# Performance work log

Hardware: AMD Instinct MI355X
Metric: run time of the kernel (lower is better)

Reference implementation:

```python
import jax, jax.numpy as jnp
import numpy as np
from jax import lax

C_RED = 32
IN_CH = 256
BN_EPS = 1e-5
NORM_EPS = 1e-6


def setup_inputs() -> dict:
    key = jax.random.key(0)
    ks = jax.random.split(key, 5)
    B, H, W = 16, 64, 64
    x = jax.random.normal(ks[0], (B, IN_CH, H, W), dtype=jnp.float32)
    w_reduce = jax.random.normal(ks[1], (C_RED, IN_CH), dtype=jnp.float32) * 0.05
    bn_gamma = jnp.ones((C_RED,), dtype=jnp.float32)
    bn_beta = jnp.zeros((C_RED,), dtype=jnp.float32)
    bn_mean = jax.random.normal(ks[2], (C_RED,), dtype=jnp.float32) * 0.1
    bn_var = jax.random.uniform(ks[3], (C_RED,), dtype=jnp.float32, minval=0.5, maxval=1.5)
    # depthwise 3x3 kernel, OIHW with I=1 (groups == channels)
    dw_weight = jax.random.normal(ks[4], (C_RED, 1, 3, 3), dtype=jnp.float32) * 0.1
    scale = jnp.ones((C_RED,), dtype=jnp.float32)
    return {"x": x, "w_reduce": w_reduce, "bn_gamma": bn_gamma, "bn_beta": bn_beta,
            "bn_mean": bn_mean, "bn_var": bn_var, "dw_weight": dw_weight, "scale": scale}


def _l2_normalize(t):
    # F.normalize(p=2, dim=1, eps=1e-6): divide by max(||t||_2, eps) along channel dim
    n = jnp.sqrt(jnp.sum(t * t, axis=1, keepdims=True))
    return t / jnp.maximum(n, NORM_EPS)


def reference(x, w_reduce, bn_gamma, bn_beta, bn_mean, bn_var, dw_weight, scale):
    # 1x1 reduce conv (no bias)
    z = jnp.einsum('bihw,oi->bohw', x, w_reduce)
    # BatchNorm2d (inference: running stats)
    inv = bn_gamma / jnp.sqrt(bn_var + BN_EPS)
    z = z * inv[None, :, None, None] + (bn_beta - bn_mean * inv)[None, :, None, None]
    z = jax.nn.relu(z)
    # SpiralTwist: depthwise 3x3 conv (SAME) then per-channel scale
    z_tw = lax.conv_general_dilated(
        z, dw_weight, window_strides=(1, 1), padding='SAME',
        feature_group_count=C_RED,
        dimension_numbers=('NCHW', 'OIHW', 'NCHW'))
    z_tw = z_tw * scale[None, :, None, None]
    z_norm = _l2_normalize(z)
    z_tw_norm = _l2_normalize(z_tw)
    # upper-triangular channel pairs (i <= j)
    idx_i, idx_j = np.triu_indices(C_RED, k=0)
    pair = z_norm[:, idx_i] * z_tw_norm[:, idx_j]  # [B, C*(C+1)/2, H, W]
    return jnp.concatenate([z_norm, pair], axis=1)
```

## Files before the change

kernel.cpp:

```cpp
#include <hip/hip_runtime.h>
#include <hip/hip_bf16.h>
#include <stdint.h>

#define HW   4096
#define CIN  256
#define CR   32
#define COUT 560

__global__ __launch_bounds__(256) void k_conv1x1(
    const float* __restrict__ x,
    const float* __restrict__ wr,
    const float* __restrict__ gamma,
    const float* __restrict__ beta,
    const float* __restrict__ mean,
    const float* __restrict__ var,
    float* __restrict__ z)
{
    const int tid = threadIdx.x;
    const int og  = __builtin_amdgcn_readfirstlane(tid >> 6);
    const int g0  = blockIdx.x * 64 + (tid & 63);
    const int b   = g0 >> 12;
    const int p   = g0 & 4095;

    const float* xb = x + ((((size_t)b) * CIN) << 12) + p;
    const float* wp = wr + (size_t)og * 8 * CIN;

    float acc[8] = {0.f,0.f,0.f,0.f,0.f,0.f,0.f,0.f};

    for (int cc = 0; cc < 16; ++cc) {
        float xv[16];
        #pragma unroll
        for (int k = 0; k < 16; ++k)
            xv[k] = xb[((size_t)(cc * 16 + k)) << 12];
        #pragma unroll
        for (int o = 0; o < 8; ++o) {
            #pragma unroll
            for (int k = 0; k < 16; ++k)
                acc[o] = fmaf(xv[k], wp[o * CIN + cc * 16 + k], acc[o]);
        }
    }

    #pragma unroll
    for (int o = 0; o < 8; ++o) {
        const int oc = og * 8 + o;
        const float inv = gamma[oc] / sqrtf(var[oc] + 1e-5f);
        const float bia = beta[oc] - mean[oc] * inv;
        z[((((size_t)b) * CR + oc) << 12) + p] =
            fmaxf(fmaf(acc[o], inv, bia), 0.f);
    }
}

__global__ __launch_bounds__(256) void k_twist(
    const float* __restrict__ z,
    const float* __restrict__ dww,
    const float* __restrict__ scl,
    float* __restrict__ out)
{
    __shared__ float dml[CR * 9];
    __shared__ float sc[CR];
    __shared__ float ps1[4 * 64];
    __shared__ float ps2[4 * 64];
    __shared__ float znl[CR * 64];
    __shared__ float twl[CR * 64];

    const int tid = threadIdx.x;
    for (int t = tid; t < CR * 9; t += 256) dml[t] = dww[t];
    if (tid < CR) sc[tid] = scl[tid];
    __syncthreads();

    const int cg  = __builtin_amdgcn_readfirstlane(tid >> 6);
    const int px  = tid & 63;
    const int g0  = blockIdx.x * 64;
    const int b   = g0 >> 12;
    const int p0  = g0 & 4095;
    const int h   = p0 >> 6;
    const float* zb = z + (((size_t)b * CR) << 12);

    float zc[8], tw[8];
    float s1 = 0.f, s2 = 0.f;
    #pragma unroll
    for (int k = 0; k < 8; ++k) {
        const int c = cg * 8 + k;
        const float* zp = zb + ((size_t)c << 12);
        float acc = 0.f, center = 0.f;
        #pragma unroll
        for (int dy = 0; dy < 3; ++dy) {
            const int hy = h + dy - 1;
            const bool rok = ((unsigned)hy) < 64u;
            #pragma unroll
            for (int dx = 0; dx < 3; ++dx) {
                const int wx = px + dx - 1;
                const bool ok = rok && (((unsigned)wx) < 64u);
                float v = 0.f;
                if (ok) v = zp[(hy << 6) + wx];
                if (dy == 1 && dx == 1) center = v;
                acc = fmaf(v, dml[c * 9 + dy * 3 + dx], acc);
            }
        }
        const float t = acc * sc[c];
        zc[k] = center; tw[k] = t;
        s1 = fmaf(center, center, s1);
        s2 = fmaf(t, t, s2);
    }
    ps1[cg * 64 + px] = s1;
    ps2[cg * 64 + px] = s2;
    __syncthreads();
    const float t1 = ps1[px] + ps1[64 + px] + ps1[128 + px] + ps1[192 + px];
    const float t2 = ps2[px] + ps2[64 + px] + ps2[128 + px] + ps2[192 + px];
    const float rn1 = 1.0f / fmaxf(sqrtf(t1), 1e-6f);
    const float rn2 = 1.0f / fmaxf(sqrtf(t2), 1e-6f);
    #pragma unroll
    for (int k = 0; k < 8; ++k) {
        znl[(cg * 8 + k) * 64 + px] = zc[k] * rn1;
        twl[(cg * 8 + k) * 64 + px] = tw[k] * rn2;
    }
    __syncthreads();

    float* outb = out + (((size_t)b * COUT) << 12) + p0 + px;
    #pragma unroll
    for (int P = 0; P < 32; ++P)
        if ((P & 3) == cg)
            outb[(size_t)P << 12] = znl[P * 64 + px];
    {
        int P = 32;
        #pragma unroll
        for (int i = 0; i < CR; ++i) {
            #pragma unroll
            for (int j = i; j < CR; ++j) {
                if ((P & 3) == cg)
                    outb[(size_t)P << 12] = znl[i * 64 + px] * twl[j * 64 + px];
                ++P;
            }
        }
    }
}

extern "C" void kernel_launch(void* const* d_in, const int* in_sizes, int n_in,
                              void* d_out, int out_size, void* d_ws, size_t ws_size,
                              hipStream_t stream) {
    const float* x     = (const float*)d_in[0];
    const float* wr    = (const float*)d_in[1];
    const float* gamma = (const float*)d_in[2];
    const float* beta  = (const float*)d_in[3];
    const float* mean  = (const float*)d_in[4];
    const float* var   = (const float*)d_in[5];
    const float* dww   = (const float*)d_in[6];
    const float* scl   = (const float*)d_in[7];
    float* z = (float*)d_ws;
    float* out = (float*)d_out;

    hipLaunchKernelGGL(k_conv1x1, dim3(1024), dim3(256), 0, stream,
                       x, wr, gamma, beta, mean, var, z);
    hipLaunchKernelGGL(k_twist, dim3(1024), dim3(256), 0, stream,
                       z, dww, scl, out);
}
```

Baseline: 240.0 us.

## Fuse 1x1 conv, BN-ReLU and depthwise twist into one kernel with halo recompute

Merges the reduce-conv kernel and the twist/pair kernel into a single kernel where each block owns one image row and recomputes the 1x1 conv for the rows above and below to form the 3x3 halo. This removes the round trip of the intermediate z tensor through global memory and one launch. It triples the conv arithmetic and input reads per block. The normalized values are also cached in registers for the pair products instead of rereading shared memory.

```diff
diff --git a/kernel.cpp b/kernel.cpp
--- a/kernel.cpp
+++ b/kernel.cpp
@@ -1,134 +1,141 @@
 #include <hip/hip_runtime.h>
-#include <hip/hip_bf16.h>
 #include <stdint.h>
 
-#define HW   4096
 #define CIN  256
 #define CR   32
 #define COUT 560
 
-__global__ __launch_bounds__(256) void k_conv1x1(
+__global__ __launch_bounds__(256, 4) void k_fused(
     const float* __restrict__ x,
     const float* __restrict__ wr,
     const float* __restrict__ gamma,
     const float* __restrict__ beta,
     const float* __restrict__ mean,
     const float* __restrict__ var,
-    float* __restrict__ z)
-{
-    const int tid = threadIdx.x;
-    const int og  = __builtin_amdgcn_readfirstlane(tid >> 6);
-    const int g0  = blockIdx.x * 64 + (tid & 63);
-    const int b   = g0 >> 12;
-    const int p   = g0 & 4095;
-
-    const float* xb = x + ((((size_t)b) * CIN) << 12) + p;
-    const float* wp = wr + (size_t)og * 8 * CIN;
-
-    float acc[8] = {0.f,0.f,0.f,0.f,0.f,0.f,0.f,0.f};
-
-    for (int cc = 0; cc < 16; ++cc) {
-        float xv[16];
-        #pragma unroll
-        for (int k = 0; k < 16; ++k)
-            xv[k] = xb[((size_t)(cc * 16 + k)) << 12];
-        #pragma unroll
-        for (int o = 0; o < 8; ++o) {
-            #pragma unroll
-            for (int k = 0; k < 16; ++k)
-                acc[o] = fmaf(xv[k], wp[o * CIN + cc * 16 + k], acc[o]);
-        }
-    }
-
-    #pragma unroll
-    for (int o = 0; o < 8; ++o) {
-        const int oc = og * 8 + o;
-        const float inv = gamma[oc] / sqrtf(var[oc] + 1e-5f);
-        const float bia = beta[oc] - mean[oc] * inv;
-        z[((((size_t)b) * CR + oc) << 12) + p] =
-            fmaxf(fmaf(acc[o], inv, bia), 0.f);
-    }
-}
-
-__global__ __launch_bounds__(256) void k_twist(
-    const float* __restrict__ z,
     const float* __restrict__ dww,
     const float* __restrict__ scl,
     float* __restrict__ out)
 {
+    __shared__ float buf[3 * CR * 64];
+    __shared__ float ps1[4 * 64], ps2[4 * 64];
     __shared__ float dml[CR * 9];
     __shared__ float sc[CR];
-    __shared__ float ps1[4 * 64];
-    __shared__ float ps2[4 * 64];
-    __shared__ float znl[CR * 64];
-    __shared__ float twl[CR * 64];
 
     const int tid = threadIdx.x;
     for (int t = tid; t < CR * 9; t += 256) dml[t] = dww[t];
     if (tid < CR) sc[tid] = scl[tid];
+
+    const int cg = __builtin_amdgcn_readfirstlane(tid >> 6);
+    const int px = tid & 63;
+    const int g  = blockIdx.x;
+    const int b  = g >> 6;
+    const int h  = g & 63;
+    const int ob = cg * 8;
+
+    float acc[3][8];
+    #pragma unroll
+    for (int r = 0; r < 3; ++r)
+        #pragma unroll
+        for (int o = 0; o < 8; ++o) acc[r][o] = 0.f;
+
+    const float* xb = x + (((size_t)b * CIN) << 12) + px;
+    const int hc0 = (h == 0)  ? 0  : h - 1;
+    const int hc2 = (h == 63) ? 63 : h + 1;
+
+    #pragma unroll 2
+    for (int c0 = 0; c0 < CIN; c0 += 8) {
+        float xv[8][3];
+        #pragma unroll
+        for (int k = 0; k < 8; ++k) {
+            const float* xp = xb + ((size_t)(c0 + k) << 12);
+            xv[k][0] = xp[hc0 << 6];
+            xv[k][1] = xp[h   << 6];
+            xv[k][2] = xp[hc2 << 6];
+        }
+        #pragma unroll
+        for (int o = 0; o < 8; ++o) {
+            const float* wp = wr + (ob + o) * CIN + c0;
+            #pragma unroll
+            for (int k = 0; k < 8; ++k) {
+                const float wv = wp[k];
+                acc[0][o] = fmaf(xv[k][0], wv, acc[0][o]);
+                acc[1][o] = fmaf(xv[k][1], wv, acc[1][o]);
+                acc[2][o] = fmaf(xv[k][2], wv, acc[2][o]);
+            }
+        }
+    }
+
+    const bool v0 = (h > 0), v2 = (h < 63);
+    float zrow[3][8];
+    #pragma unroll
+    for (int o = 0; o < 8; ++o) {
+        const int oc = ob + o;
+        const float inv = gamma[oc] / sqrtf(var[oc] + 1e-5f);
+        const float bia = beta[oc] - mean[oc] * inv;
+        zrow[0][o] = v0 ? fmaxf(fmaf(acc[0][o], inv, bia), 0.f) : 0.f;
+        zrow[1][o] =      fmaxf(fmaf(acc[1][o], inv, bia), 0.f);
+        zrow[2][o] = v2 ? fmaxf(fmaf(acc[2][o], inv, bia), 0.f) : 0.f;
+    }
+    #pragma unroll
+    for (int r = 0; r < 3; ++r)
+        #pragma unroll
+        for (int o = 0; o < 8; ++o)
+            buf[((r * CR) + ob + o) * 64 + px] = zrow[r][o];
     __syncthreads();
 
-    const int cg  = __builtin_amdgcn_readfirstlane(tid >> 6);
-    const int px  = tid & 63;
-    const int g0  = blockIdx.x * 64;
-    const int b   = g0 >> 12;
-    const int p0  = g0 & 4095;
-    const int h   = p0 >> 6;
-    const float* zb = z + (((size_t)b * CR) << 12);
-
-    float zc[8], tw[8];
+    float twv[8], zcv[8];
     float s1 = 0.f, s2 = 0.f;
     #pragma unroll
     for (int k = 0; k < 8; ++k) {
-        const int c = cg * 8 + k;
-        const float* zp = zb + ((size_t)c << 12);
-        float acc = 0.f, center = 0.f;
+        const int c = ob + k;
+        float a = 0.f;
         #pragma unroll
-        for (int dy = 0; dy < 3; ++dy) {
-            const int hy = h + dy - 1;
-            const bool rok = ((unsigned)hy) < 64u;
-            #pragma unroll
-            for (int dx = 0; dx < 3; ++dx) {
-                const int wx = px + dx - 1;
-                const bool ok = rok && (((unsigned)wx) < 64u);
-                float v = 0.f;
-                if (ok) v = zp[(hy << 6) + wx];
-                if (dy == 1 && dx == 1) center = v;
-                acc = fmaf(v, dml[c * 9 + dy * 3 + dx], acc);
-            }
+        for (int r = 0; r < 3; ++r) {
+            const float* zp = &buf[(r * CR + c) * 64];
+            const float vL = (px > 0)  ? zp[px - 1] : 0.f;
+            const float vC =             zp[px];
+            const float vR = (px < 63) ? zp[px + 1] : 0.f;
+            a = fmaf(vL, dml[c * 9 + r * 3 + 0], a);
+            a = fmaf(vC, dml[c * 9 + r * 3 + 1], a);
+            a = fmaf(vR, dml[c * 9 + r * 3 + 2], a);
         }
-        const float t = acc * sc[c];
-        zc[k] = center; tw[k] = t;
-        s1 = fmaf(center, center, s1);
+        const float t = a * sc[c];
+        twv[k] = t;
+        zcv[k] = zrow[1][k];
+        s1 = fmaf(zcv[k], zcv[k], s1);
         s2 = fmaf(t, t, s2);
     }
     ps1[cg * 64 + px] = s1;
     ps2[cg * 64 + px] = s2;
     __syncthreads();
-    const float t1 = ps1[px] + ps1[64 + px] + ps1[128 + px] + ps1[192 + px];
-    const float t2 = ps2[px] + ps2[64 + px] + ps2[128 + px] + ps2[192 + px];
-    const float rn1 = 1.0f / fmaxf(sqrtf(t1), 1e-6f);
-    const float rn2 = 1.0f / fmaxf(sqrtf(t2), 1e-6f);
+    const float rn1 = 1.f / fmaxf(sqrtf(ps1[px] + ps1[64 + px] + ps1[128 + px] + ps1[192 + px]), 1e-6f);
+    const float rn2 = 1.f / fmaxf(sqrtf(ps2[px] + ps2[64 + px] + ps2[128 + px] + ps2[192 + px]), 1e-6f);
+
     #pragma unroll
     for (int k = 0; k < 8; ++k) {
-        znl[(cg * 8 + k) * 64 + px] = zc[k] * rn1;
-        twl[(cg * 8 + k) * 64 + px] = tw[k] * rn2;
+        buf[(ob + k) * 64 + px]        = zcv[k] * rn1;
+        buf[2048 + (ob + k) * 64 + px] = twv[k] * rn2;
     }
     __syncthreads();
 
-    float* outb = out + (((size_t)b * COUT) << 12) + p0 + px;
+    float zn[CR], tw[CR];
     #pragma unroll
-    for (int P = 0; P < 32; ++P)
-        if ((P & 3) == cg)
-            outb[(size_t)P << 12] = znl[P * 64 + px];
+    for (int c = 0; c < CR; ++c) {
+        zn[c] = buf[c * 64 + px];
+        tw[c] = buf[2048 + c * 64 + px];
+    }
+
+    float* outb = out + (((size_t)b * COUT) << 12) + (h << 6) + px;
+    #pragma unroll
+    for (int P = 0; P < CR; ++P)
+        if ((P & 3) == cg) outb[(size_t)P << 12] = zn[P];
     {
-        int P = 32;
+        int P = CR;
         #pragma unroll
         for (int i = 0; i < CR; ++i) {
             #pragma unroll
             for (int j = i; j < CR; ++j) {
-                if ((P & 3) == cg)
-                    outb[(size_t)P << 12] = znl[i * 64 + px] * twl[j * 64 + px];
+                if ((P & 3) == cg) outb[(size_t)P << 12] = zn[i] * tw[j];
                 ++P;
             }
         }
@@ -146,11 +153,8 @@
     const float* var   = (const float*)d_in[5];
     const float* dww   = (const float*)d_in[6];
     const float* scl   = (const float*)d_in[7];
-    float* z = (float*)d_ws;
     float* out = (float*)d_out;
 
-    hipLaunchKernelGGL(k_conv1x1, dim3(1024), dim3(256), 0, stream,
-                       x, wr, gamma, beta, mean, var, z);
-    hipLaunchKernelGGL(k_twist, dim3(1024), dim3(256), 0, stream,
-                       z, dww, scl, out);
+    hipLaunchKernelGGL(k_fused, dim3(1024), dim3(256), 0, stream,
+                       x, wr, gamma, beta, mean, var, dww, scl, out);
 }
```

Result: slower. 269.3 us (+12.2%).
